# Performance work log

Hardware: AMD Instinct MI355X
Metric: run time of the kernel (lower is better)

## Reference

```python
import jax, jax.numpy as jnp
import numpy as np
from jax import lax

B, N, D = 8, 16384, 64
NPOINT, NSAMPLE, RADIUS = 1024, 32, 0.1
MLP = [3 + D, 64, 64, 128]
BN_EPS = 1e-5


def setup_inputs() -> dict:
    key = jax.random.key(0)
    ks = jax.random.split(key, 8)
    inp = {
        'xyz': jax.random.uniform(ks[0], (B, 3, N), dtype=jnp.float32),
        'points': jax.random.normal(ks[1], (B, D, N), dtype=jnp.float32),
    }
    for i, (cin, cout) in enumerate(zip(MLP[:-1], MLP[1:]), start=1):
        inp[f'w{i}'] = jax.random.normal(ks[1 + i], (cout, cin), dtype=jnp.float32) / np.sqrt(cin)
        inp[f'b{i}'] = jnp.zeros((cout,), jnp.float32)
        inp[f'g{i}'] = jnp.ones((cout,), jnp.float32)
        inp[f'be{i}'] = jnp.zeros((cout,), jnp.float32)
    return inp


def farthest_point_sample(xyz, npoint):
    # xyz: (B, N, 3). Deterministic start at index 0 (torch uses randint).
    b, n, _ = xyz.shape

    def step(carry, _):
        distance, farthest = carry  # (B,N), (B,)
        centroid = jnp.take_along_axis(xyz, farthest[:, None, None], axis=1)  # (B,1,3)
        dist = jnp.sum((xyz - centroid) ** 2, axis=-1)  # (B,N)
        distance = jnp.minimum(distance, dist)
        new_far = jnp.argmax(distance, axis=-1).astype(jnp.int32)
        return (distance, new_far), farthest

    init = (jnp.full((b, n), 1e10, xyz.dtype), jnp.zeros((b,), jnp.int32))
    _, idxs = lax.scan(step, init, None, length=npoint)  # (npoint, B)
    return idxs.T  # (B, npoint)


def query_ball_point(radius, nsample, xyz, new_xyz):
    # xyz: (B,N,3), new_xyz: (B,S,3) -> (B,S,nsample) int32
    b, n, _ = xyz.shape
    # squared pairwise distances (B,S,N)
    sqr = (jnp.sum(new_xyz ** 2, -1)[:, :, None]
           + jnp.sum(xyz ** 2, -1)[:, None, :]
           - 2.0 * jnp.einsum('bsc,bnc->bsn', new_xyz, xyz))
    group_idx = jnp.where(sqr > radius ** 2, n, jnp.arange(n, dtype=jnp.int32))
    group_idx = jnp.sort(group_idx, axis=-1)[:, :, :nsample]
    first = group_idx[:, :, :1]
    return jnp.where(group_idx == n, first, group_idx)


def reference(xyz, points, w1, b1, g1, be1, w2, b2, g2, be2, w3, b3, g3, be3):
    xyz_t = xyz.transpose(0, 2, 1)      # (B,N,3)
    pts_t = points.transpose(0, 2, 1)   # (B,N,D)
    bsz = xyz_t.shape[0]

    fps_idx = farthest_point_sample(xyz_t, NPOINT)          # (B,S)
    bidx2 = jnp.arange(bsz)[:, None]
    new_xyz = xyz_t[bidx2, fps_idx]                          # (B,S,3)

    idx = query_ball_point(RADIUS, NSAMPLE, xyz_t, new_xyz)  # (B,S,ns)
    bidx3 = jnp.arange(bsz)[:, None, None]
    grouped_xyz = xyz_t[bidx3, idx] - new_xyz[:, :, None, :]  # (B,S,ns,3)
    grouped_pts = pts_t[bidx3, idx]                           # (B,S,ns,D)
    feat = jnp.concatenate([grouped_xyz, grouped_pts], axis=-1)  # (B,S,ns,C)

    for w, b, g, be in ((w1, b1, g1, be1), (w2, b2, g2, be2), (w3, b3, g3, be3)):
        feat = jnp.einsum('bsnc,oc->bsno', feat, w) + b
        mean = feat.mean(axis=(0, 1, 2))
        var = feat.var(axis=(0, 1, 2))  # biased, as torch BN uses for normalization
        feat = (feat - mean) * lax.rsqrt(var + BN_EPS) * g + be
        feat = jax.nn.relu(feat)

    new_points = feat.max(axis=2)  # max over nsample -> (B,S,Cout)
    return new_xyz.transpose(0, 2, 1), new_points.transpose(0, 2, 1)
```

## Files before the change

kernel.cpp:

```cpp
#include <hip/hip_runtime.h>
#include <hip/hip_bf16.h>
#include <stdint.h>

#define BATCH 8
#define NPTS  16384
#define DIMF  64
#define SPTS  1024
#define NSAMP 32
#define MTOT  (BATCH*SPTS*NSAMP)

__device__ __forceinline__ float bfu_lo(uint32_t u){ return __uint_as_float(u<<16); }
__device__ __forceinline__ float bfu_hi(uint32_t u){ return __uint_as_float(u & 0xffff0000u); }
__device__ __forceinline__ uint16_t f2bf(float f){
  __hip_bfloat16 h = __float2bfloat16(f);
  uint16_t u; __builtin_memcpy(&u, &h, 2); return u;
}

__global__ __launch_bounds__(256) void transpose_kernel(const float* __restrict__ pts,
                                                        float* __restrict__ ptsT){
  __shared__ float tile[32][33];
  int b = blockIdx.z;
  int n0 = blockIdx.x*32, c0 = blockIdx.y*32;
  int tx = threadIdx.x & 31, ty = threadIdx.x >> 5;
  const float* src = pts + (size_t)b*DIMF*NPTS;
  float* dst = ptsT + (size_t)b*NPTS*DIMF;
#pragma unroll
  for (int j=0;j<4;j++)
    tile[ty+8*j][tx] = src[(size_t)(c0+ty+8*j)*NPTS + n0 + tx];
  __syncthreads();
#pragma unroll
  for (int j=0;j<4;j++)
    dst[(size_t)(n0+ty+8*j)*DIMF + c0 + tx] = tile[tx][ty+8*j];
}

__global__ __launch_bounds__(1024) void fps_kernel(const float* __restrict__ xyz,
                                                   float* __restrict__ out0){
  int b = blockIdx.x;
  const float* X = xyz + (size_t)b*3*NPTS;
  int t = threadIdx.x;
  int lane = t & 63, wid = t >> 6;
  float px[16], py[16], pz[16], dst[16];
#pragma unroll
  for (int k=0;k<16;k++){
    int n = t + (k<<10);
    px[k]=X[n]; py[k]=X[NPTS+n]; pz[k]=X[2*NPTS+n];
    dst[k]=1e10f;
  }
  __shared__ float rv[16];
  __shared__ int   ri[16];
  __shared__ int   far_sh;
  int far = 0;
  float* o = out0 + (size_t)b*3*SPTS;
  for (int s=0;s<SPTS;s++){
    float cx = X[far], cy = X[NPTS+far], cz = X[2*NPTS+far];
    if (t==0){ o[s]=cx; o[SPTS+s]=cy; o[2*SPTS+s]=cz; }
    if (s==SPTS-1) break;
    float best = -1.0f; int bi = 0x7fffffff;
#pragma unroll
    for (int k=0;k<16;k++){
      float dx=__fsub_rn(px[k],cx), dy=__fsub_rn(py[k],cy), dz=__fsub_rn(pz[k],cz);
      float d = __fadd_rn(__fadd_rn(__fmul_rn(dx,dx),__fmul_rn(dy,dy)),__fmul_rn(dz,dz));
      d = fminf(dst[k], d); dst[k] = d;
      if (d > best){ best = d; bi = t + (k<<10); }
    }
#pragma unroll
    for (int off=1; off<64; off<<=1){
      float ov = __shfl_xor(best, off);
      int   oi = __shfl_xor(bi, off);
      if (ov > best || (ov == best && oi < bi)){ best = ov; bi = oi; }
    }
    if (lane==0){ rv[wid]=best; ri[wid]=bi; }
    __syncthreads();
    if (wid==0){
      float v = (lane<16) ? rv[lane] : -2.0f;
      int   j = (lane<16) ? ri[lane] : 0x7fffffff;
#pragma unroll
      for (int off=1; off<16; off<<=1){
        float ov = __shfl_xor(v, off);
        int   oi = __shfl_xor(j, off);
        if (ov > v || (ov == v && oi < j)){ v = ov; j = oi; }
      }
      if (lane==0) far_sh = j;
    }
    __syncthreads();
    far = far_sh;
  }
}

__global__ __launch_bounds__(256) void ball_kernel(const float* __restrict__ xyz,
                                                   const float* __restrict__ newxyz,
                                                   int* __restrict__ idxo){
  int b  = blockIdx.x >> 5;
  int sc = blockIdx.x & 31;
  const float* X  = xyz + (size_t)b*3*NPTS;
  int t = threadIdx.x, lane = t & 63, w = t >> 6;
  __shared__ float lx[512], ly[512], lz[512], ls[512];
  __shared__ int done;
  if (t==0) done = 0;
  const float rsq = 0.01f;
  float nx[8], ny[8], nz[8], sn[8];
  int cnt[8], first[8];
  int sbase = sc*32 + w*8;
#pragma unroll
  for (int q=0;q<8;q++){
    int s = sbase + q;
    nx[q] = newxyz[(size_t)b*3*SPTS + s];
    ny[q] = newxyz[(size_t)b*3*SPTS + SPTS + s];
    nz[q] = newxyz[(size_t)b*3*SPTS + 2*SPTS + s];
    sn[q] = __fadd_rn(__fadd_rn(__fmul_rn(nx[q],nx[q]),__fmul_rn(ny[q],ny[q])),
                      __fmul_rn(nz[q],nz[q]));
    cnt[q]=0; first[q]=0;
  }
  __syncthreads();
  for (int T=0;T<32;T++){
    {
      float ax = X[T*512 + t], ay = X[NPTS + T*512 + t], az = X[2*NPTS + T*512 + t];
      lx[t]=ax; ly[t]=ay; lz[t]=az;
      ls[t] = __fadd_rn(__fadd_rn(__fmul_rn(ax,ax),__fmul_rn(ay,ay)),__fmul_rn(az,az));
      float bx = X[T*512 + t + 256], by = X[NPTS + T*512 + t + 256], bz = X[2*NPTS + T*512 + t + 256];
      lx[t+256]=bx; ly[t+256]=by; lz[t+256]=bz;
      ls[t+256] = __fadd_rn(__fadd_rn(__fmul_rn(bx,bx),__fmul_rn(by,by)),__fmul_rn(bz,bz));
    }
    __syncthreads();
#pragma unroll
    for (int q=0;q<8;q++){
      if (cnt[q] >= NSAMP) continue;
      int s = sbase + q;
      int* op = idxo + ((size_t)(b*SPTS + s))*NSAMP;
      for (int c=0;c<8;c++){
        int li = c*64 + lane;
        float dot = fmaf(nz[q], lz[li], fmaf(ny[q], ly[li], __fmul_rn(nx[q], lx[li])));
        float sq  = __fsub_rn(__fadd_rn(sn[q], ls[li]), __fmul_rn(2.0f, dot));
        bool in = (sq <= rsq);
        unsigned long long m = __ballot(in);
        if (cnt[q]==0 && m) first[q] = T*512 + c*64 + (int)__builtin_ctzll(m);
        if (in){
          int slot = cnt[q] + (int)__popcll(m & ((1ull<<lane)-1ull));
          if (slot < NSAMP) op[slot] = T*512 + li;
        }
        cnt[q] += (int)__popcll(m);
        if (cnt[q] >= NSAMP){ if (lane==0) atomicAdd(&done,1); break; }
      }
    }
    __syncthreads();
    if (done >= 32) break;
  }
#pragma unroll
  for (int q=0;q<8;q++){
    if (cnt[q] < NSAMP){
      int s = sbase + q;
      int* op = idxo + ((size_t)(b*SPTS + s))*NSAMP;
      if (lane >= cnt[q] && lane < NSAMP) op[lane] = first[q];
    }
  }
}

__global__ __launch_bounds__(256) void gemm1_kernel(const float* __restrict__ xyz,
                                                    const float* __restrict__ ptsT,
                                                    const int* __restrict__ idx,
                                                    const float* __restrict__ newxyz,
                                                    const float* __restrict__ w1,
                                                    const float* __restrict__ b1,
                                                    uint16_t* __restrict__ y1){
  __shared__ float As[128*69];
  __shared__ float Ws[67*64];
  __shared__ float bias[64];
  __shared__ int   ndx[128];
  __shared__ float nxs[4][3];
  int t = threadIdx.x;
  int g0 = blockIdx.x*128;
  if (t < 128) ndx[t] = idx[g0 + t];
  if (t < 12){
    int grp = t/3, c = t%3;
    int bs = (g0>>5) + grp; int b = bs>>10, s = bs & 1023;
    nxs[grp][c] = newxyz[(size_t)b*3*SPTS + c*SPTS + s];
  }
  if (t < 64) bias[t] = b1[t];
  for (int e=t; e<67*64; e+=256){ int k=e>>6, c=e&63; Ws[k*64+c] = w1[c*67+k]; }
  __syncthreads();
  {
    int r = t>>1, h = t&1;
    int n = ndx[r];
    int bs = (g0>>5) + (r>>5); int b = bs>>10;
    const float* pr = ptsT + ((size_t)(b*NPTS + n))*64 + h*32;
    float* ar = As + r*69;
    if (h==0){
      int grp = r>>5;
      ar[0] = __fsub_rn(xyz[(size_t)b*3*NPTS + n],          nxs[grp][0]);
      ar[1] = __fsub_rn(xyz[(size_t)b*3*NPTS + NPTS + n],   nxs[grp][1]);
      ar[2] = __fsub_rn(xyz[(size_t)b*3*NPTS + 2*NPTS + n], nxs[grp][2]);
    }
    float* ap = ar + 3 + h*32;
#pragma unroll
    for (int j=0;j<8;j++){
      float4 v = *(const float4*)(pr + j*4);
      ap[j*4+0]=v.x; ap[j*4+1]=v.y; ap[j*4+2]=v.z; ap[j*4+3]=v.w;
    }
  }
  __syncthreads();
  int rg = t>>3, cg = t&7;
  float acc[4][8];
#pragma unroll
  for (int i=0;i<4;i++)
#pragma unroll
    for (int j=0;j<8;j++) acc[i][j]=0.f;
  for (int k=0;k<67;k++){
    float a0 = As[(rg*4+0)*69+k];
    float a1 = As[(rg*4+1)*69+k];
    float a2 = As[(rg*4+2)*69+k];
    float a3 = As[(rg*4+3)*69+k];
    const float* wr = Ws + k*64 + cg*8;
    float4 w0 = *(const float4*)wr;
    float4 w1v = *(const float4*)(wr+4);
    float wj[8] = {w0.x,w0.y,w0.z,w0.w,w1v.x,w1v.y,w1v.z,w1v.w};
#pragma unroll
    for (int j=0;j<8;j++){
      acc[0][j] = fmaf(a0, wj[j], acc[0][j]);
      acc[1][j] = fmaf(a1, wj[j], acc[1][j]);
      acc[2][j] = fmaf(a2, wj[j], acc[2][j]);
      acc[3][j] = fmaf(a3, wj[j], acc[3][j]);
    }
  }
#pragma unroll
  for (int i=0;i<4;i++){
    int gr = g0 + rg*4 + i;
    uint16_t* yr = y1 + (size_t)gr*64 + cg*8;
    uint4 vv;
    uint32_t u[4];
#pragma unroll
    for (int j=0;j<4;j++){
      float v0 = acc[i][2*j]   + bias[cg*8+2*j];
      float v1 = acc[i][2*j+1] + bias[cg*8+2*j+1];
      u[j] = (uint32_t)f2bf(v0) | ((uint32_t)f2bf(v1)<<16);
    }
    vv.x=u[0]; vv.y=u[1]; vv.z=u[2]; vv.w=u[3];
    *(uint4*)yr = vv;
  }
}

__global__ __launch_bounds__(256) void gemm2_kernel(const uint16_t* __restrict__ yin,
                                                    const float* __restrict__ w2,
                                                    const float* __restrict__ b2,
                                                    const float* __restrict__ scale,
                                                    const float* __restrict__ shift,
                                                    uint16_t* __restrict__ yout){
  __shared__ float As[128*65];
  __shared__ float Ws[64*64];
  __shared__ float bias[64], sc[64], sh[64];
  int t = threadIdx.x;
  int g0 = blockIdx.x*128;
  if (t < 64){ bias[t]=b2[t]; sc[t]=scale[t]; sh[t]=shift[t]; }
  for (int e=t; e<64*64; e+=256){ int k=e>>6, c=e&63; Ws[k*64+c] = w2[c*64+k]; }
  __syncthreads();
  {
    int r = t>>1, h = t&1;
    const uint4* yv = (const uint4*)(yin + (size_t)(g0+r)*64 + h*32);
    float* ar = As + r*65 + h*32;
#pragma unroll
    for (int j=0;j<4;j++){
      uint4 u = yv[j];
      uint32_t vv[4] = {u.x,u.y,u.z,u.w};
#pragma unroll
      for (int m=0;m<4;m++){
        int c = h*32 + j*8 + m*2;
        ar[j*8+m*2]   = fmaxf(fmaf(bfu_lo(vv[m]), sc[c],   sh[c]),   0.f);
        ar[j*8+m*2+1] = fmaxf(fmaf(bfu_hi(vv[m]), sc[c+1], sh[c+1]), 0.f);
      }
    }
  }
  __syncthreads();
  int rg = t>>3, cg = t&7;
  float acc[4][8];
#pragma unroll
  for (int i=0;i<4;i++)
#pragma unroll
    for (int j=0;j<8;j++) acc[i][j]=0.f;
  for (int k=0;k<64;k++){
    float a0 = As[(rg*4+0)*65+k];
    float a1 = As[(rg*4+1)*65+k];
    float a2 = As[(rg*4+2)*65+k];
    float a3 = As[(rg*4+3)*65+k];
    const float* wr = Ws + k*64 + cg*8;
    float4 w0 = *(const float4*)wr;
    float4 w1v = *(const float4*)(wr+4);
    float wj[8] = {w0.x,w0.y,w0.z,w0.w,w1v.x,w1v.y,w1v.z,w1v.w};
#pragma unroll
    for (int j=0;j<8;j++){
      acc[0][j] = fmaf(a0, wj[j], acc[0][j]);
      acc[1][j] = fmaf(a1, wj[j], acc[1][j]);
      acc[2][j] = fmaf(a2, wj[j], acc[2][j]);
      acc[3][j] = fmaf(a3, wj[j], acc[3][j]);
    }
  }
#pragma unroll
  for (int i=0;i<4;i++){
    int gr = g0 + rg*4 + i;
    uint16_t* yr = yout + (size_t)gr*64 + cg*8;
    uint4 vv; uint32_t u[4];
#pragma unroll
    for (int j=0;j<4;j++){
      float v0 = acc[i][2*j]   + bias[cg*8+2*j];
      float v1 = acc[i][2*j+1] + bias[cg*8+2*j+1];
      u[j] = (uint32_t)f2bf(v0) | ((uint32_t)f2bf(v1)<<16);
    }
    vv.x=u[0]; vv.y=u[1]; vv.z=u[2]; vv.w=u[3];
    *(uint4*)yr = vv;
  }
}

__global__ __launch_bounds__(256) void gemm3_kernel(const uint16_t* __restrict__ yin,
                                                    const float* __restrict__ w3,
                                                    const float* __restrict__ b3,
                                                    const float* __restrict__ scale,
                                                    const float* __restrict__ shift,
                                                    uint16_t* __restrict__ yout){
  __shared__ float As[64*65];
  __shared__ float Ws[64*128];
  __shared__ float bias[128], sc[64], sh[64];
  int t = threadIdx.x;
  int g0 = blockIdx.x*64;
  if (t < 128) bias[t]=b3[t];
  if (t < 64){ sc[t]=scale[t]; sh[t]=shift[t]; }
  for (int e=t; e<64*128; e+=256){ int k=e>>7, c=e&127; Ws[k*128+c] = w3[c*64+k]; }
  __syncthreads();
  {
    int r = t>>2, h = t&3;
    const uint4* yv = (const uint4*)(yin + (size_t)(g0+r)*64 + h*16);
    float* ar = As + r*65 + h*16;
#pragma unroll
    for (int j=0;j<2;j++){
      uint4 u = yv[j];
      uint32_t vv[4] = {u.x,u.y,u.z,u.w};
#pragma unroll
      for (int m=0;m<4;m++){
        int c = h*16 + j*8 + m*2;
        ar[j*8+m*2]   = fmaxf(fmaf(bfu_lo(vv[m]), sc[c],   sh[c]),   0.f);
        ar[j*8+m*2+1] = fmaxf(fmaf(bfu_hi(vv[m]), sc[c+1], sh[c+1]), 0.f);
      }
    }
  }
  __syncthreads();
  int rg = t>>4, cg = t&15;
  float acc[4][8];
#pragma unroll
  for (int i=0;i<4;i++)
#pragma unroll
    for (int j=0;j<8;j++) acc[i][j]=0.f;
  for (int k=0;k<64;k++){
    float a0 = As[(rg*4+0)*65+k];
    float a1 = As[(rg*4+1)*65+k];
    float a2 = As[(rg*4+2)*65+k];
    float a3 = As[(rg*4+3)*65+k];
    const float* wr = Ws + k*128 + cg*8;
    float4 w0 = *(const float4*)wr;
    float4 w1v = *(const float4*)(wr+4);
    float wj[8] = {w0.x,w0.y,w0.z,w0.w,w1v.x,w1v.y,w1v.z,w1v.w};
#pragma unroll
    for (int j=0;j<8;j++){
      acc[0][j] = fmaf(a0, wj[j], acc[0][j]);
      acc[1][j] = fmaf(a1, wj[j], acc[1][j]);
      acc[2][j] = fmaf(a2, wj[j], acc[2][j]);
      acc[3][j] = fmaf(a3, wj[j], acc[3][j]);
    }
  }
#pragma unroll
  for (int i=0;i<4;i++){
    int gr = g0 + rg*4 + i;
    uint16_t* yr = yout + (size_t)gr*128 + cg*8;
    uint4 vv; uint32_t u[4];
#pragma unroll
    for (int j=0;j<4;j++){
      float v0 = acc[i][2*j]   + bias[cg*8+2*j];
      float v1 = acc[i][2*j+1] + bias[cg*8+2*j+1];
      u[j] = (uint32_t)f2bf(v0) | ((uint32_t)f2bf(v1)<<16);
    }
    vv.x=u[0]; vv.y=u[1]; vv.z=u[2]; vv.w=u[3];
    *(uint4*)yr = vv;
  }
}

template<int C>
__global__ __launch_bounds__(256) void stats_kernel(const uint16_t* __restrict__ y,
                                                    float* __restrict__ gsum,
                                                    float* __restrict__ gsq){
  constexpr int CP  = C/2;
  constexpr int RSL = 256/CP;
  int t = threadIdx.x;
  int c0 = t % CP, rs = t / CP;
  float s0=0.f,q0=0.f,s1=0.f,q1=0.f;
#pragma unroll 4
  for (int i=0;i<512/RSL;i++){
    int r = blockIdx.x*512 + rs + i*RSL;
    uint32_t u = *(const uint32_t*)(y + (size_t)r*C + 2*c0);
    float v0 = bfu_lo(u), v1 = bfu_hi(u);
    s0 += v0; q0 += v0*v0; s1 += v1; q1 += v1*v1;
  }
  __shared__ float red[4][256];
  red[0][t]=s0; red[1][t]=q0; red[2][t]=s1; red[3][t]=q1;
  __syncthreads();
  if (t < CP){
    float a0=0,a1=0,a2=0,a3=0;
    for (int k=0;k<RSL;k++){
      a0+=red[0][k*CP+t]; a1+=red[1][k*CP+t]; a2+=red[2][k*CP+t]; a3+=red[3][k*CP+t];
    }
    atomicAdd(&gsum[2*t],   a0); atomicAdd(&gsq[2*t],   a1);
    atomicAdd(&gsum[2*t+1], a2); atomicAdd(&gsq[2*t+1], a3);
  }
}

__global__ void finalize_kernel(const float* __restrict__ gsum, const float* __restrict__ gsq,
                                const float* __restrict__ g, const float* __restrict__ be,
                                float* __restrict__ scale, float* __restrict__ shift, int C){
  int c = threadIdx.x;
  if (c >= C) return;
  double mean = (double)gsum[c] / (double)MTOT;
  double var  = (double)gsq[c] / (double)MTOT - mean*mean;
  double s    = (double)g[c] / sqrt(var + 1e-5);
  scale[c] = (float)s;
  shift[c] = (float)((double)be[c] - mean*s);
}

__global__ __launch_bounds__(256) void maxpool_kernel(const uint16_t* __restrict__ y3,
                                                      const float* __restrict__ scale,
                                                      const float* __restrict__ shift,
                                                      float* __restrict__ out1){
  __shared__ float tr[16][129];
  int t = threadIdx.x;
  int b = blockIdx.x >> 6;
  int s0 = (blockIdx.x & 63) * 16;
  int ch = t & 127, sl0 = t >> 7;
  float scv = scale[ch], shv = shift[ch];
  for (int sl=sl0; sl<16; sl+=2){
    int bs = b*SPTS + s0 + sl;
    const uint16_t* yr = y3 + (size_t)bs*NSAMP*128 + ch;
    float m = 0.0f;
#pragma unroll 4
    for (int k=0;k<NSAMP;k++){
      float v = __uint_as_float(((uint32_t)yr[k*128])<<16);
      float z = fmaxf(fmaf(v, scv, shv), 0.f);
      m = fmaxf(m, z);
    }
    tr[sl][ch] = m;
  }
  __syncthreads();
  int ch2 = t >> 1, hh = t & 1;
  float vals[8];
#pragma unroll
  for (int i=0;i<8;i++) vals[i] = tr[hh*8+i][ch2];
  float* op = out1 + (size_t)b*131072 + (size_t)ch2*1024 + s0 + hh*8;
  float4 v0; v0.x=vals[0]; v0.y=vals[1]; v0.z=vals[2]; v0.w=vals[3];
  float4 v1; v1.x=vals[4]; v1.y=vals[5]; v1.z=vals[6]; v1.w=vals[7];
  *(float4*)op = v0;
  *(float4*)(op+4) = v1;
}

extern "C" void kernel_launch(void* const* d_in, const int* in_sizes, int n_in,
                              void* d_out, int out_size, void* d_ws, size_t ws_size,
                              hipStream_t stream){
  (void)in_sizes; (void)n_in; (void)out_size; (void)ws_size;
  const float* xyz = (const float*)d_in[0];
  const float* pts = (const float*)d_in[1];
  const float* w1 = (const float*)d_in[2];  const float* b1 = (const float*)d_in[3];
  const float* g1 = (const float*)d_in[4];  const float* be1 = (const float*)d_in[5];
  const float* w2 = (const float*)d_in[6];  const float* b2 = (const float*)d_in[7];
  const float* g2 = (const float*)d_in[8];  const float* be2 = (const float*)d_in[9];
  const float* w3 = (const float*)d_in[10]; const float* b3 = (const float*)d_in[11];
  const float* g3 = (const float*)d_in[12]; const float* be3 = (const float*)d_in[13];

  float* out0 = (float*)d_out;
  float* out1 = out0 + BATCH*3*SPTS;

  char* ws = (char*)d_ws;
  float*    ptsT = (float*)(ws + 0);
  int*      idx  = (int*)  (ws + 34078720);
  uint16_t* y1   = (uint16_t*)(ws + 35127296);
  uint16_t* y2   = (uint16_t*)(ws + 68681728);
  uint16_t* y3   = (uint16_t*)(ws + 102236160);
  float*    stats = (float*)(ws + 169345024);
  float* gsum1 = stats;        float* gsq1 = stats + 128;
  float* gsum2 = stats + 256;  float* gsq2 = stats + 384;
  float* gsum3 = stats + 512;  float* gsq3 = stats + 640;
  float* scale1 = stats + 768; float* shift1 = stats + 896;
  float* scale2 = stats + 1024; float* shift2 = stats + 1152;
  float* scale3 = stats + 1280; float* shift3 = stats + 1408;

  hipMemsetAsync(stats, 0, 768*sizeof(float), stream);

  transpose_kernel<<<dim3(NPTS/32, DIMF/32, BATCH), 256, 0, stream>>>(pts, ptsT);
  fps_kernel<<<BATCH, 1024, 0, stream>>>(xyz, out0);
  ball_kernel<<<BATCH*32, 256, 0, stream>>>(xyz, out0, idx);
  gemm1_kernel<<<MTOT/128, 256, 0, stream>>>(xyz, ptsT, idx, out0, w1, b1, y1);
  stats_kernel<64><<<512, 256, 0, stream>>>(y1, gsum1, gsq1);
  finalize_kernel<<<1, 128, 0, stream>>>(gsum1, gsq1, g1, be1, scale1, shift1, 64);
  gemm2_kernel<<<MTOT/128, 256, 0, stream>>>(y1, w2, b2, scale1, shift1, y2);
  stats_kernel<64><<<512, 256, 0, stream>>>(y2, gsum2, gsq2);
  finalize_kernel<<<1, 128, 0, stream>>>(gsum2, gsq2, g2, be2, scale2, shift2, 64);
  gemm3_kernel<<<MTOT/64, 256, 0, stream>>>(y2, w3, b3, scale2, shift2, y3);
  stats_kernel<128><<<512, 256, 0, stream>>>(y3, gsum3, gsq3);
  finalize_kernel<<<1, 128, 0, stream>>>(gsum3, gsq3, g3, be3, scale3, shift3, 128);
  maxpool_kernel<<<BATCH*(SPTS/16), 256, 0, stream>>>(y3, scale3, shift3, out1);
}
```

Measured before the change: 2.817 ms.

## Cut FPS barriers with redundant per-wave reduction and carried centroid coordinates

The farthest-point-sampling loop now carries the winning point's coordinates through the shuffle reductions, so the next centroid no longer needs a dependent global load. Every wave redundantly performs the final 16-way reduction from double-buffered shared slots, which removes the second __syncthreads per iteration. x/y coordinates move from registers into a 128KB shared array to lower register pressure. The cost is more shuffles per step, extra shared-memory reads in the inner loop, and heavy LDS use that limits the block to one per CU.

```diff
diff --git a/kernel.cpp b/kernel.cpp
--- a/kernel.cpp
+++ b/kernel.cpp
@@ -39,51 +39,60 @@
   const float* X = xyz + (size_t)b*3*NPTS;
   int t = threadIdx.x;
   int lane = t & 63, wid = t >> 6;
-  float px[16], py[16], pz[16], dst[16];
+  __shared__ float2 lxy[NPTS];
+  __shared__ float4 rr[2][16];
+  __shared__ int    rj[2][16];
+  float pz[16], dst[16];
 #pragma unroll
   for (int k=0;k<16;k++){
     int n = t + (k<<10);
-    px[k]=X[n]; py[k]=X[NPTS+n]; pz[k]=X[2*NPTS+n];
-    dst[k]=1e10f;
-  }
-  __shared__ float rv[16];
-  __shared__ int   ri[16];
-  __shared__ int   far_sh;
-  int far = 0;
+    float2 xy; xy.x = X[n]; xy.y = X[NPTS+n];
+    lxy[n] = xy;
+    pz[k]  = X[2*NPTS+n];
+    dst[k] = 1e10f;
+  }
+  float cx = X[0], cy = X[NPTS], cz = X[2*NPTS];
+  __syncthreads();
   float* o = out0 + (size_t)b*3*SPTS;
   for (int s=0;s<SPTS;s++){
-    float cx = X[far], cy = X[NPTS+far], cz = X[2*NPTS+far];
     if (t==0){ o[s]=cx; o[SPTS+s]=cy; o[2*SPTS+s]=cz; }
     if (s==SPTS-1) break;
     float best = -1.0f; int bi = 0x7fffffff;
+    float bx=0.f, by=0.f, bz=0.f;
 #pragma unroll
     for (int k=0;k<16;k++){
-      float dx=__fsub_rn(px[k],cx), dy=__fsub_rn(py[k],cy), dz=__fsub_rn(pz[k],cz);
+      int n = t + (k<<10);
+      float2 xy = lxy[n];
+      float dx=__fsub_rn(xy.x,cx), dy=__fsub_rn(xy.y,cy), dz=__fsub_rn(pz[k],cz);
       float d = __fadd_rn(__fadd_rn(__fmul_rn(dx,dx),__fmul_rn(dy,dy)),__fmul_rn(dz,dz));
       d = fminf(dst[k], d); dst[k] = d;
-      if (d > best){ best = d; bi = t + (k<<10); }
+      if (d > best){ best=d; bi=n; bx=xy.x; by=xy.y; bz=pz[k]; }
     }
 #pragma unroll
     for (int off=1; off<64; off<<=1){
       float ov = __shfl_xor(best, off);
-      int   oi = __shfl_xor(bi, off);
-      if (ov > best || (ov == best && oi < bi)){ best = ov; bi = oi; }
-    }
-    if (lane==0){ rv[wid]=best; ri[wid]=bi; }
+      int   oj = __shfl_xor(bi,  off);
+      float ox = __shfl_xor(bx,  off);
+      float oy = __shfl_xor(by,  off);
+      float oz = __shfl_xor(bz,  off);
+      bool take = (ov > best) || (ov == best && oj < bi);
+      if (take){ best=ov; bi=oj; bx=ox; by=oy; bz=oz; }
+    }
+    int p = s & 1;
+    if (lane==0){ rr[p][wid] = make_float4(bx,by,bz,best); rj[p][wid] = bi; }
     __syncthreads();
-    if (wid==0){
-      float v = (lane<16) ? rv[lane] : -2.0f;
-      int   j = (lane<16) ? ri[lane] : 0x7fffffff;
-#pragma unroll
-      for (int off=1; off<16; off<<=1){
-        float ov = __shfl_xor(v, off);
-        int   oi = __shfl_xor(j, off);
-        if (ov > v || (ov == v && oi < j)){ v = ov; j = oi; }
-      }
-      if (lane==0) far_sh = j;
-    }
-    __syncthreads();
-    far = far_sh;
+    float4 q = rr[p][lane&15]; int j = rj[p][lane&15];
+#pragma unroll
+    for (int off=1; off<16; off<<=1){
+      float ow = __shfl_xor(q.w, off);
+      int   oj = __shfl_xor(j,   off);
+      float ox = __shfl_xor(q.x, off);
+      float oy = __shfl_xor(q.y, off);
+      float oz = __shfl_xor(q.z, off);
+      bool take = (ow > q.w) || (ow == q.w && oj < j);
+      if (take){ q.w=ow; j=oj; q.x=ox; q.y=oy; q.z=oz; }
+    }
+    cx = q.x; cy = q.y; cz = q.z;
   }
 }
 
```

After: 3.859 ms. 1.37x slower.

## Accelerate farthest point sampling with spatial grid cells and bound-based pruning

Applied to the files above, without the earlier changes.

Farthest point sampling now bins points into an 8x8x8 grid, sorted into workspace arrays, and keeps per-cell max distance. Each iteration rescans only the cells whose lower-bound distance to the new centroid could lower their current max, then picks the global max from the per-cell maxima. This replaces the full scan of all 16384 points per step with sparse cell updates, at the cost of atomics, shared-memory distance arrays, and a conservative float bound that must keep results identical to the reference.

```diff
diff --git a/kernel.cpp b/kernel.cpp
--- a/kernel.cpp
+++ b/kernel.cpp
@@ -8,6 +8,7 @@
 #define SPTS  1024
 #define NSAMP 32
 #define MTOT  (BATCH*SPTS*NSAMP)
+#define CELLS 512
 
 __device__ __forceinline__ float bfu_lo(uint32_t u){ return __uint_as_float(u<<16); }
 __device__ __forceinline__ float bfu_hi(uint32_t u){ return __uint_as_float(u & 0xffff0000u); }
@@ -33,57 +34,146 @@
     dst[(size_t)(n0+ty+8*j)*DIMF + c0 + tx] = tile[tx][ty+8*j];
 }
 
+__device__ __forceinline__ int cell_of(float x, float y, float z){
+  int ix=(int)(x*8.0f); ix = ix<0?0:(ix>7?7:ix);
+  int iy=(int)(y*8.0f); iy = iy<0?0:(iy>7?7:iy);
+  int iz=(int)(z*8.0f); iz = iz<0?0:(iz>7?7:iz);
+  return (ix<<6)|(iy<<3)|iz;
+}
+
 __global__ __launch_bounds__(1024) void fps_kernel(const float* __restrict__ xyz,
-                                                   float* __restrict__ out0){
+                                                   float* __restrict__ out0,
+                                                   float* __restrict__ sxg,
+                                                   float* __restrict__ syg,
+                                                   float* __restrict__ szg,
+                                                   int*   __restrict__ sidg){
   int b = blockIdx.x;
   const float* X = xyz + (size_t)b*3*NPTS;
+  float* sx = sxg + b*NPTS;  float* sy = syg + b*NPTS;
+  float* sz = szg + b*NPTS;  int*   sid = sidg + b*NPTS;
   int t = threadIdx.x;
   int lane = t & 63, wid = t >> 6;
-  float px[16], py[16], pz[16], dst[16];
+
+  __shared__ float dst_s[NPTS];
+  __shared__ int   hist[CELLS];
+  __shared__ int   cstart[CELLS];
+  __shared__ int   cursor[CELLS];
+  __shared__ float cmaxv[CELLS];
+  __shared__ int   cmaxk[CELLS];
+  __shared__ float cwx[CELLS], cwy[CELLS], cwz[CELLS];
+  __shared__ int   dlist[CELLS];
+  __shared__ int   ndirty;
+  __shared__ int   wsum[16];
+  __shared__ float pv[16]; __shared__ int pk[16];
+
+  if (t < CELLS) hist[t] = 0;
+  __syncthreads();
 #pragma unroll
   for (int k=0;k<16;k++){
     int n = t + (k<<10);
-    px[k]=X[n]; py[k]=X[NPTS+n]; pz[k]=X[2*NPTS+n];
-    dst[k]=1e10f;
-  }
-  __shared__ float rv[16];
-  __shared__ int   ri[16];
-  __shared__ int   far_sh;
-  int far = 0;
+    atomicAdd(&hist[cell_of(X[n], X[NPTS+n], X[2*NPTS+n])], 1);
+  }
+  __syncthreads();
+  {
+    int v = (t<CELLS)? hist[t] : 0;
+    int inc = v;
+#pragma unroll
+    for (int off=1; off<64; off<<=1){
+      int u = __shfl_up(inc, off);
+      if (lane >= off) inc += u;
+    }
+    if (t<CELLS && lane==63) wsum[wid] = inc;
+    __syncthreads();
+    if (t==0){ int acc=0; for(int w=0;w<8;w++){ int x=wsum[w]; wsum[w]=acc; acc+=x; } }
+    __syncthreads();
+    if (t<CELLS){
+      int ex = inc - v + wsum[wid];
+      cstart[t]=ex; cursor[t]=ex; cmaxv[t]=1e10f; cmaxk[t]=0x3fff;
+    }
+  }
+  __syncthreads();
+#pragma unroll
+  for (int k=0;k<16;k++){
+    int n = t + (k<<10);
+    float x=X[n], y=X[NPTS+n], z=X[2*NPTS+n];
+    int c = cell_of(x,y,z);
+    int pos = atomicAdd(&cursor[c],1);
+    sx[pos]=x; sy[pos]=y; sz[pos]=z; sid[pos]=n;
+  }
+  for (int n=t; n<NPTS; n+=1024) dst_s[n]=1e10f;
+  if (t==0) ndirty=0;
+  __syncthreads();
+
+  float cx=X[0], cy=X[NPTS], cz=X[2*NPTS];
   float* o = out0 + (size_t)b*3*SPTS;
   for (int s=0;s<SPTS;s++){
-    float cx = X[far], cy = X[NPTS+far], cz = X[2*NPTS+far];
     if (t==0){ o[s]=cx; o[SPTS+s]=cy; o[2*SPTS+s]=cz; }
     if (s==SPTS-1) break;
-    float best = -1.0f; int bi = 0x7fffffff;
-#pragma unroll
-    for (int k=0;k<16;k++){
-      float dx=__fsub_rn(px[k],cx), dy=__fsub_rn(py[k],cy), dz=__fsub_rn(pz[k],cz);
-      float d = __fadd_rn(__fadd_rn(__fmul_rn(dx,dx),__fmul_rn(dy,dy)),__fmul_rn(dz,dz));
-      d = fminf(dst[k], d); dst[k] = d;
-      if (d > best){ best = d; bi = t + (k<<10); }
-    }
-#pragma unroll
-    for (int off=1; off<64; off<<=1){
-      float ov = __shfl_xor(best, off);
-      int   oi = __shfl_xor(bi, off);
-      if (ov > best || (ov == best && oi < bi)){ best = ov; bi = oi; }
-    }
-    if (lane==0){ rv[wid]=best; ri[wid]=bi; }
+    if (t < CELLS){
+      float lox = (t>>6)      * 0.125f;
+      float loy = ((t>>3)&7)  * 0.125f;
+      float loz = (t&7)       * 0.125f;
+      float dxx = fmaxf(fmaxf(lox-cx, cx-(lox+0.125f)), 0.f);
+      float dyy = fmaxf(fmaxf(loy-cy, cy-(loy+0.125f)), 0.f);
+      float dzz = fmaxf(fmaxf(loz-cz, cz-(loz+0.125f)), 0.f);
+      float lb  = dxx*dxx + dyy*dyy + dzz*dzz;
+      float lbAdj = lb*(1.0f-4e-6f) - 4e-6f;
+      if (lbAdj < cmaxv[t]){
+        int p = atomicAdd(&ndirty,1);
+        dlist[p] = t;
+      }
+    }
     __syncthreads();
-    if (wid==0){
-      float v = (lane<16) ? rv[lane] : -2.0f;
-      int   j = (lane<16) ? ri[lane] : 0x7fffffff;
+    int nd = ndirty;
+    for (int i=wid; i<nd; i+=16){
+      int c  = dlist[i];
+      int st = cstart[c];
+      int en = (c==CELLS-1)? NPTS : cstart[c+1];
+      float bv=-1.f; int bo=0x7fffffff; float bx=0.f, by=0.f, bz=0.f;
+      for (int base=st; base<en; base+=64){
+        int pos = base+lane;
+        if (pos<en){
+          float x=sx[pos], y=sy[pos], z=sz[pos];
+          float od = dst_s[pos];
+          float ddx=__fsub_rn(x,cx), ddy=__fsub_rn(y,cy), ddz=__fsub_rn(z,cz);
+          float d = __fadd_rn(__fadd_rn(__fmul_rn(ddx,ddx),__fmul_rn(ddy,ddy)),
+                              __fmul_rn(ddz,ddz));
+          d = fminf(od, d);
+          dst_s[pos] = d;
+          int orig = sid[pos];
+          if (d > bv || (d == bv && orig < bo)){ bv=d; bo=orig; bx=x; by=y; bz=z; }
+        }
+      }
+#pragma unroll
+      for (int off=1; off<64; off<<=1){
+        float ov=__shfl_xor(bv,off); int oo=__shfl_xor(bo,off);
+        float ox=__shfl_xor(bx,off), oy=__shfl_xor(by,off), oz=__shfl_xor(bz,off);
+        if (ov>bv || (ov==bv && oo<bo)){ bv=ov; bo=oo; bx=ox; by=oy; bz=oz; }
+      }
+      if (lane==0){ cmaxv[c]=bv; cmaxk[c]=bo; cwx[c]=bx; cwy[c]=by; cwz[c]=bz; }
+    }
+    __syncthreads();
+    {
+      float v; int key;
+      if (t < CELLS){ v = cmaxv[t]; key = ((cmaxk[t]&0x3fff)<<9) | t; }
+      else          { v = -2.f;     key = 0x7fffffff; }
+#pragma unroll
+      for (int off=1; off<64; off<<=1){
+        float ov=__shfl_xor(v,off); int ok=__shfl_xor(key,off);
+        if (ov>v || (ov==v && ok<key)){ v=ov; key=ok; }
+      }
+      if (lane==0){ pv[wid]=v; pk[wid]=key; }
+      if (t==0) ndirty = 0;
+      __syncthreads();
+      v = pv[lane&15]; key = pk[lane&15];
 #pragma unroll
       for (int off=1; off<16; off<<=1){
-        float ov = __shfl_xor(v, off);
-        int   oi = __shfl_xor(j, off);
-        if (ov > v || (ov == v && oi < j)){ v = ov; j = oi; }
-      }
-      if (lane==0) far_sh = j;
-    }
-    __syncthreads();
-    far = far_sh;
+        float ov=__shfl_xor(v,off); int ok=__shfl_xor(key,off);
+        if (ov>v || (ov==v && ok<key)){ v=ov; key=ok; }
+      }
+      int cell = key & 511;
+      cx = cwx[cell]; cy = cwy[cell]; cz = cwz[cell];
+    }
   }
 }
 
@@ -477,6 +567,10 @@
   uint16_t* y2   = (uint16_t*)(ws + 68681728);
   uint16_t* y3   = (uint16_t*)(ws + 102236160);
   float*    stats = (float*)(ws + 169345024);
+  float* sxg = (float*)(ws + 35127296);
+  float* syg = (float*)(ws + 35127296 +   524288);
+  float* szg = (float*)(ws + 35127296 + 2*524288);
+  int*   sidg= (int*)  (ws + 35127296 + 3*524288);
   float* gsum1 = stats;        float* gsq1 = stats + 128;
   float* gsum2 = stats + 256;  float* gsq2 = stats + 384;
   float* gsum3 = stats + 512;  float* gsq3 = stats + 640;
@@ -487,7 +581,7 @@
   hipMemsetAsync(stats, 0, 768*sizeof(float), stream);
 
   transpose_kernel<<<dim3(NPTS/32, DIMF/32, BATCH), 256, 0, stream>>>(pts, ptsT);
-  fps_kernel<<<BATCH, 1024, 0, stream>>>(xyz, out0);
+  fps_kernel<<<BATCH, 1024, 0, stream>>>(xyz, out0, sxg, syg, szg, sidg);
   ball_kernel<<<BATCH*32, 256, 0, stream>>>(xyz, out0, idx);
   gemm1_kernel<<<MTOT/128, 256, 0, stream>>>(xyz, ptsT, idx, out0, w1, b1, y1);
   stats_kernel<64><<<512, 256, 0, stream>>>(y1, gsum1, gsq1);
```

Result: slower. 4.014 ms (+42.5%).
